# Kernel optimization log

Measured on AMD Instinct MI355X. Metric: run time of the kernel, lower is better.

Reference implementation:

```python
import jax, jax.numpy as jnp
import numpy as np
from jax import lax

NUM_TAGS = 126
T = NUM_TAGS + 2          # tag_size = 128
B, S = 256, 512
START, STOP = T - 3, T - 2
NEG = -10000.0


def setup_inputs() -> dict:
    key = jax.random.key(0)
    k1, k2, k3 = jax.random.split(key, 3)
    feats = jax.random.normal(k1, (B, S, T), jnp.float32)
    # learned transition matrix with the module's init masking pattern
    trans = jax.random.normal(k2, (T, T), jnp.float32)
    trans = trans.at[:, START].set(NEG).at[STOP, :].set(NEG)
    trans = trans.at[:, 0].set(NEG).at[0, :].set(NEG)
    # prefix masks with varying valid lengths in [S/2, S]
    lengths = jax.random.randint(k3, (B,), S // 2, S + 1)
    mask = jnp.arange(S)[None, :] < lengths[:, None]
    return {"feats": feats, "mask": mask, "transitions": trans}


def reference(feats, mask, transitions):
    # Viterbi decode (module.forward returns (None, decode_idx)).
    Bn, Sn, Tn = feats.shape
    start, stop = Tn - 3, Tn - 2
    emit = jnp.transpose(feats, (1, 0, 2))            # (S, B, T)
    m = jnp.transpose(mask.astype(jnp.int32))         # (S, B)
    lengths = mask.astype(jnp.int32).sum(axis=1)      # (B,)

    part0 = emit[0] + transitions[start][None, :]     # (B, T)

    def step(part, inp):
        e_t, m_t = inp
        # scores[t, b, i, j] = feats[t, b, j] + transitions[i, j]
        cur = part[:, :, None] + transitions[None, :, :] + e_t[:, None, :]  # (B, from, to)
        new_part = cur.max(axis=1)                                          # (B, T)
        bp = jnp.argmax(cur, axis=1).astype(jnp.int32)                      # (B, T)
        bp = jnp.where(m_t[:, None] > 0, bp, 0)
        return new_part, (new_part, bp)

    _, (hist, bps) = lax.scan(step, part0, (emit[1:], m[1:]))
    part_hist = jnp.concatenate([part0[None], hist], axis=0)                # (S, B, T)
    back_points = jnp.concatenate(
        [bps, jnp.zeros((1, Bn, Tn), jnp.int32)], axis=0)                   # (S, B, T)

    bidx = jnp.arange(Bn)
    last_pos = lengths - 1                                                  # (B,)
    last_partition = part_hist[last_pos, bidx]                              # (B, T)
    last_bp = jnp.argmax(last_partition[:, :, None] + transitions[None], axis=1)
    pointer = last_bp[:, stop].astype(jnp.int32)                            # (B,)

    # overwrite back_points at the last valid position with the final pointer
    bp_bt = jnp.transpose(back_points, (1, 0, 2))                           # (B, S, T)
    bp_bt = bp_bt.at[bidx, last_pos].set(
        jnp.broadcast_to(pointer[:, None], (Bn, Tn)))
    back_points = jnp.transpose(bp_bt, (1, 0, 2))                           # (S, B, T)

    def trace(ptr, bp_t):
        new_ptr = jnp.take_along_axis(bp_t, ptr[:, None], axis=1)[:, 0]
        return new_ptr, new_ptr

    _, rev = lax.scan(trace, pointer, back_points[:-1], reverse=True)       # (S-1, B)
    decode = jnp.concatenate([rev, pointer[None]], axis=0)                  # (S, B)
    return jnp.transpose(decode)                                            # (B, S)
```

## Files before the change

### kernel.cpp

```cpp
#include <hip/hip_runtime.h>
#include <cstdint>
#include <cstddef>

constexpr int T_ = 128;
constexpr int S_ = 512;
constexpr int B_ = 256;
constexpr int START_ = T_ - 3;
constexpr int STOP_  = T_ - 2;
constexpr float NEGINF_ = -3.402823466e38f;

__device__ __forceinline__ void lds_barrier() {
  asm volatile("s_waitcnt lgkmcnt(0)\n\ts_barrier" ::: "memory");
}

__device__ __forceinline__ float readlane_f(float v, int sl) {
  return __int_as_float(__builtin_amdgcn_readlane(__float_as_int(v), sl));
}

__device__ __forceinline__ float ig_reduce_max(float m) {
  int x = __builtin_amdgcn_mov_dpp(__float_as_int(m), 0xB1, 0xF, 0xF, true);
  m = fmaxf(m, __int_as_float(x));
  x = __builtin_amdgcn_mov_dpp(__float_as_int(m), 0x4E, 0xF, 0xF, true);
  m = fmaxf(m, __int_as_float(x));
  x = __builtin_amdgcn_mov_dpp(__float_as_int(m), 0x141, 0xF, 0xF, true);
  m = fmaxf(m, __int_as_float(x));
  return m;
}

__global__ __launch_bounds__(256) void viterbi_forward(
    const float* __restrict__ feats,
    const float* __restrict__ trans,
    float* __restrict__ ph)
{
  const int tid  = threadIdx.x;
  const int lane = tid & 63;
  const int w    = tid >> 6;
  const int ig   = lane & 7;
  const int jl   = lane >> 3;
  const int jg   = w * 8 + jl;
  const int j0   = jg * 4;
  const int b    = blockIdx.x;

  __shared__ alignas(16) float part[2][160];

  float4 tc[16];
  #pragma unroll
  for (int ii = 0; ii < 16; ++ii)
    tc[ii] = *(const float4*)&trans[(16 * ig + ii) * T_ + j0];

  const float* fb = feats + (size_t)b * S_ * T_;
  const int woff = j0 + 4 * (jg >> 2);

  float4 e0 = *(const float4*)&fb[j0];
  float4 ts = *(const float4*)&trans[START_ * T_ + j0];
  float4 p0 = make_float4(e0.x + ts.x, e0.y + ts.y, e0.z + ts.z, e0.w + ts.w);
  if (ig == 0) {
    *(float4*)&part[0][woff] = p0;
    *(float4*)&ph[(size_t)b * T_ + j0] = p0;
  }
  float4 e_next = *(const float4*)&fb[T_ + j0];
  __syncthreads();

  for (int t = 1; t < S_; ++t) {
    float4 e_cur = e_next;
    if (t + 1 < S_) e_next = *(const float4*)&fb[(size_t)(t + 1) * T_ + j0];

    const float4* p4 = (const float4*)part[(t - 1) & 1];
    float4 p[4];
    #pragma unroll
    for (int q = 0; q < 4; ++q) p[q] = p4[5 * ig + q];

    float m0 = NEGINF_, m1 = NEGINF_, m2 = NEGINF_, m3 = NEGINF_;
    #pragma unroll
    for (int q = 0; q < 4; ++q) {
      float4 pv = p[q];
      float4 t0 = tc[4 * q + 0], t1 = tc[4 * q + 1];
      float4 t2 = tc[4 * q + 2], t3 = tc[4 * q + 3];
      m0 = fmaxf(m0, fmaxf(fmaxf(pv.x + t0.x, pv.y + t1.x),
                           fmaxf(pv.z + t2.x, pv.w + t3.x)));
      m1 = fmaxf(m1, fmaxf(fmaxf(pv.x + t0.y, pv.y + t1.y),
                           fmaxf(pv.z + t2.y, pv.w + t3.y)));
      m2 = fmaxf(m2, fmaxf(fmaxf(pv.x + t0.z, pv.y + t1.z),
                           fmaxf(pv.z + t2.z, pv.w + t3.z)));
      m3 = fmaxf(m3, fmaxf(fmaxf(pv.x + t0.w, pv.y + t1.w),
                           fmaxf(pv.z + t2.w, pv.w + t3.w)));
    }
    float4 np4 = make_float4(ig_reduce_max(m0) + e_cur.x,
                             ig_reduce_max(m1) + e_cur.y,
                             ig_reduce_max(m2) + e_cur.z,
                             ig_reduce_max(m3) + e_cur.w);
    if (ig == 0) *(float4*)&part[t & 1][woff] = np4;
    lds_barrier();
    if (ig == 0)
      *(float4*)&ph[((size_t)t * B_ + b) * T_ + j0] = np4;
  }
}

constexpr int CH_ = 8;
constexpr int TS_ = 130;

__global__ __launch_bounds__(64) void viterbi_trace(
    const float* __restrict__ feats,
    const void*  __restrict__ mask,
    const float* __restrict__ trans,
    const float* __restrict__ ph,
    int* __restrict__ out)
{
  const int b    = blockIdx.x;
  const int lane = threadIdx.x;

  __shared__ alignas(16) float transT[T_ * TS_];
  #pragma unroll 4
  for (int g = lane; g < T_ * T_; g += 64) {
    int i = g >> 7, jj = g & (T_ - 1);
    transT[jj * TS_ + i] = trans[g];
  }
  __syncthreads();

  int len = 0;
  {
    const int w0 = *(const int*)mask;
    if (w0 == 0x01010101) {
      const unsigned char* m = (const unsigned char*)mask + (size_t)b * S_;
      for (int s = lane; s < S_; s += 64) len += (m[s] != 0);
    } else if (w0 == 0x3F800000) {
      const float* m = (const float*)mask + (size_t)b * S_;
      for (int s = lane; s < S_; s += 64) len += (m[s] != 0.0f);
    } else {
      const int* m = (const int*)mask + (size_t)b * S_;
      for (int s = lane; s < S_; s += 64) len += (m[s] != 0);
    }
    #pragma unroll
    for (int o = 32; o > 0; o >>= 1) len += __shfl_xor(len, o);
  }
  const int lp = len - 1;

  const float2 L = *(const float2*)(ph + ((size_t)lp * B_ + b) * T_ + 2 * lane);
  float v0 = L.x + transT[STOP_ * TS_ + 2 * lane];
  float v1 = L.y + transT[STOP_ * TS_ + 2 * lane + 1];
  float mx = fmaxf(v0, v1);
  #pragma unroll
  for (int o = 32; o > 0; o >>= 1) mx = fmaxf(mx, __shfl_xor(mx, o));
  {
    unsigned long long g0 = __ballot(v0 == mx);
    unsigned long long g1 = __ballot(v1 == mx);
    int p0 = g0 ? 2 * (__ffsll(g0) - 1)     : (1 << 30);
    int p1 = g1 ? 2 * (__ffsll(g1) - 1) + 1 : (1 << 30);
    int pointer = min(p0, p1);

    for (int k = lp + 1 + lane; k <= S_ - 2; k += 64) out[b * S_ + k] = 0;
    if (lane == 0) {
      out[b * S_ + (S_ - 1)] = pointer;
      if (lp < S_ - 1) out[b * S_ + lp] = pointer;
    }

    int   ptr = pointer;
    float tg  = readlane_f((ptr & 1) ? L.y : L.x, ptr >> 1);
    const float* fb = feats + (size_t)b * S_ * T_;
    const float2 FL = *(const float2*)(fb + (size_t)lp * T_ + 2 * lane);
    float e = readlane_f((ptr & 1) ? FL.y : FL.x, ptr >> 1);

    float2 PA[CH_], FA[CH_], PB[CH_], FB[CH_];

    auto issue = [&](float2 (&P)[CH_], float2 (&F)[CH_], int k0) {
      #pragma unroll
      for (int s = 0; s < CH_; ++s) {
        int k = k0 - s; if (k < 0) k = 0;
        P[s] = *(const float2*)(ph + ((size_t)k * B_ + b) * T_ + 2 * lane);
        F[s] = *(const float2*)(fb + (size_t)k * T_ + 2 * lane);
      }
    };
    auto process = [&](const float2 (&P)[CH_], const float2 (&F)[CH_], int k0) {
      #pragma unroll
      for (int s = 0; s < CH_; ++s) {
        const int k = k0 - s;
        if (k >= 0) {
          const float2 tr = *(const float2*)(transT + ptr * TS_ + 2 * lane);
          float cx = (P[s].x + tr.x) + e;
          float cy = (P[s].y + tr.y) + e;
          unsigned long long q0 = __ballot(cx == tg);
          unsigned long long q1 = __ballot(cy == tg);
          int a0 = q0 ? 2 * (__ffsll(q0) - 1)     : (1 << 30);
          int a1 = q1 ? 2 * (__ffsll(q1) - 1) + 1 : (1 << 30);
          ptr = min(a0, a1);
          if (lane == 0) out[b * S_ + k] = ptr;
          tg = readlane_f((ptr & 1) ? P[s].y : P[s].x, ptr >> 1);
          e  = readlane_f((ptr & 1) ? F[s].y : F[s].x, ptr >> 1);
        }
      }
    };

    issue(PA, FA, lp - 1);
    for (int k0 = lp - 1; k0 >= 0; k0 -= 2 * CH_) {
      issue(PB, FB, k0 - CH_);
      process(PA, FA, k0);
      issue(PA, FA, k0 - 2 * CH_);
      process(PB, FB, k0 - CH_);
    }
  }
}

extern "C" void kernel_launch(void* const* d_in, const int* in_sizes, int n_in,
                              void* d_out, int out_size, void* d_ws, size_t ws_size,
                              hipStream_t stream) {
  const float* feats = (const float*)d_in[0];
  const void*  mask  = d_in[1];
  const float* trans = (const float*)d_in[2];
  float* ph = (float*)d_ws;
  int*   out = (int*)d_out;

  viterbi_forward<<<dim3(B_), dim3(256), 0, stream>>>(feats, trans, ph);
  viterbi_trace  <<<dim3(B_), dim3(64), 0, stream>>>(feats, mask, trans, ph, out);
}
```

Before: 455.4 us.

## Store byte backpointers in forward pass and trace them from LDS

```diff
diff --git a/kernel.cpp b/kernel.cpp
--- a/kernel.cpp
+++ b/kernel.cpp
@@ -7,17 +7,12 @@
 constexpr int B_ = 256;
 constexpr int START_ = T_ - 3;
 constexpr int STOP_  = T_ - 2;
-constexpr float NEGINF_ = -3.402823466e38f;
 
 __device__ __forceinline__ void lds_barrier() {
   asm volatile("s_waitcnt lgkmcnt(0)\n\ts_barrier" ::: "memory");
 }
 
-__device__ __forceinline__ float readlane_f(float v, int sl) {
-  return __int_as_float(__builtin_amdgcn_readlane(__float_as_int(v), sl));
-}
-
-__device__ __forceinline__ float ig_reduce_max(float m) {
+__device__ __forceinline__ float ig_rmax(float m) {
   int x = __builtin_amdgcn_mov_dpp(__float_as_int(m), 0xB1, 0xF, 0xF, true);
   m = fmaxf(m, __int_as_float(x));
   x = __builtin_amdgcn_mov_dpp(__float_as_int(m), 0x4E, 0xF, 0xF, true);
@@ -26,12 +21,24 @@
   m = fmaxf(m, __int_as_float(x));
   return m;
 }
+__device__ __forceinline__ int ig_rmin(int m) {
+  int x = __builtin_amdgcn_mov_dpp(m, 0xB1, 0xF, 0xF, true);
+  m = min(m, x);
+  x = __builtin_amdgcn_mov_dpp(m, 0x4E, 0xF, 0xF, true);
+  m = min(m, x);
+  x = __builtin_amdgcn_mov_dpp(m, 0x141, 0xF, 0xF, true);
+  m = min(m, x);
+  return m;
+}
 
 __global__ __launch_bounds__(256) void viterbi_forward(
     const float* __restrict__ feats,
     const float* __restrict__ trans,
-    float* __restrict__ ph)
+    const void*  __restrict__ mask,
+    unsigned int* __restrict__ bp4,
+    float* __restrict__ lastpart)
 {
+  const int b    = blockIdx.x;
   const int tid  = threadIdx.x;
   const int lane = tid & 63;
   const int w    = tid >> 6;
@@ -39,83 +46,146 @@
   const int jl   = lane >> 3;
   const int jg   = w * 8 + jl;
   const int j0   = jg * 4;
-  const int b    = blockIdx.x;
+  const int ig16 = ig * 16;
 
   __shared__ alignas(16) float part[2][160];
-
-  float4 tc[16];
+  __shared__ int lensh[4];
+
+  float tcc[4][16];
   #pragma unroll
-  for (int ii = 0; ii < 16; ++ii)
-    tc[ii] = *(const float4*)&trans[(16 * ig + ii) * T_ + j0];
-
-  const float* fb = feats + (size_t)b * S_ * T_;
-  const int woff = j0 + 4 * (jg >> 2);
-
-  float4 e0 = *(const float4*)&fb[j0];
-  float4 ts = *(const float4*)&trans[START_ * T_ + j0];
-  float4 p0 = make_float4(e0.x + ts.x, e0.y + ts.y, e0.z + ts.z, e0.w + ts.w);
-  if (ig == 0) {
-    *(float4*)&part[0][woff] = p0;
-    *(float4*)&ph[(size_t)b * T_ + j0] = p0;
-  }
-  float4 e_next = *(const float4*)&fb[T_ + j0];
+  for (int ii = 0; ii < 16; ++ii) {
+    float4 v = *(const float4*)&trans[(ig16 + ii) * T_ + j0];
+    tcc[0][ii] = v.x; tcc[1][ii] = v.y; tcc[2][ii] = v.z; tcc[3][ii] = v.w;
+  }
+
+  int cnt = 0;
+  {
+    const int w0 = *(const int*)mask;
+    if (w0 == 0x01010101) {
+      const unsigned char* m = (const unsigned char*)mask + (size_t)b * S_;
+      cnt = (m[tid] != 0) + (m[tid + 256] != 0);
+    } else if (w0 == 0x3F800000) {
+      const float* m = (const float*)mask + (size_t)b * S_;
+      cnt = (m[tid] != 0.0f) + (m[tid + 256] != 0.0f);
+    } else {
+      const int* m = (const int*)mask + (size_t)b * S_;
+      cnt = (m[tid] != 0) + (m[tid + 256] != 0);
+    }
+    #pragma unroll
+    for (int o = 32; o > 0; o >>= 1) cnt += __shfl_xor(cnt, o);
+    if (lane == 0) lensh[w] = cnt;
+  }
+
+  const float* fb   = feats + (size_t)b * S_ * T_;
+  const int    woff = j0 + 4 * (jg >> 2);
+
+  float4 e0v = *(const float4*)&fb[j0];
+  float4 tsv = *(const float4*)&trans[START_ * T_ + j0];
+  float4 p0  = {e0v.x + tsv.x, e0v.y + tsv.y, e0v.z + tsv.z, e0v.w + tsv.w};
+  if (ig == 0) *(float4*)&part[0][woff] = p0;
   __syncthreads();
-
-  for (int t = 1; t < S_; ++t) {
-    float4 e_cur = e_next;
-    if (t + 1 < S_) e_next = *(const float4*)&fb[(size_t)(t + 1) * T_ + j0];
-
+  const int lp = lensh[0] + lensh[1] + lensh[2] + lensh[3] - 1;
+
+  auto stepf = [&](int t, float4 e4) {
     const float4* p4 = (const float4*)part[(t - 1) & 1];
-    float4 p[4];
-    #pragma unroll
-    for (int q = 0; q < 4; ++q) p[q] = p4[5 * ig + q];
-
-    float m0 = NEGINF_, m1 = NEGINF_, m2 = NEGINF_, m3 = NEGINF_;
+    float pp[16];
     #pragma unroll
     for (int q = 0; q < 4; ++q) {
-      float4 pv = p[q];
-      float4 t0 = tc[4 * q + 0], t1 = tc[4 * q + 1];
-      float4 t2 = tc[4 * q + 2], t3 = tc[4 * q + 3];
-      m0 = fmaxf(m0, fmaxf(fmaxf(pv.x + t0.x, pv.y + t1.x),
-                           fmaxf(pv.z + t2.x, pv.w + t3.x)));
-      m1 = fmaxf(m1, fmaxf(fmaxf(pv.x + t0.y, pv.y + t1.y),
-                           fmaxf(pv.z + t2.y, pv.w + t3.y)));
-      m2 = fmaxf(m2, fmaxf(fmaxf(pv.x + t0.z, pv.y + t1.z),
-                           fmaxf(pv.z + t2.z, pv.w + t3.z)));
-      m3 = fmaxf(m3, fmaxf(fmaxf(pv.x + t0.w, pv.y + t1.w),
-                           fmaxf(pv.z + t2.w, pv.w + t3.w)));
-    }
-    float4 np4 = make_float4(ig_reduce_max(m0) + e_cur.x,
-                             ig_reduce_max(m1) + e_cur.y,
-                             ig_reduce_max(m2) + e_cur.z,
-                             ig_reduce_max(m3) + e_cur.w);
+      float4 v = p4[5 * ig + q];
+      pp[4*q] = v.x; pp[4*q+1] = v.y; pp[4*q+2] = v.z; pp[4*q+3] = v.w;
+    }
+    const float ev[4] = {e4.x, e4.y, e4.z, e4.w};
+    float np[4]; int bpk[4];
+    #pragma unroll
+    for (int c = 0; c < 4; ++c) {
+      float v8[8]; int i8[8];
+      #pragma unroll
+      for (int a = 0; a < 8; ++a) {
+        float da = (pp[2*a]     + tcc[c][2*a])     + ev[c];
+        float db = (pp[2*a + 1] + tcc[c][2*a + 1]) + ev[c];
+        bool s = da >= db;
+        v8[a] = s ? da : db; i8[a] = s ? (2*a) : (2*a + 1);
+      }
+      float v4[4]; int i4[4];
+      #pragma unroll
+      for (int a = 0; a < 4; ++a) {
+        bool s = v8[2*a] >= v8[2*a + 1];
+        v4[a] = s ? v8[2*a] : v8[2*a + 1]; i4[a] = s ? i8[2*a] : i8[2*a + 1];
+      }
+      float v2[2]; int i2[2];
+      #pragma unroll
+      for (int a = 0; a < 2; ++a) {
+        bool s = v2[0] >= 0;
+        (void)s;
+        bool ss = v4[2*a] >= v4[2*a + 1];
+        v2[a] = ss ? v4[2*a] : v4[2*a + 1]; i2[a] = ss ? i4[2*a] : i4[2*a + 1];
+      }
+      bool s0 = v2[0] >= v2[1];
+      float cv = s0 ? v2[0] : v2[1];
+      int   ci = s0 ? i2[0] : i2[1];
+      float M = ig_rmax(cv);
+      int key = (cv == M) ? (ig16 + ci) : 255;
+      key = ig_rmin(key);
+      np[c] = M; bpk[c] = key;
+    }
+    float4 np4 = {np[0], np[1], np[2], np[3]};
     if (ig == 0) *(float4*)&part[t & 1][woff] = np4;
     lds_barrier();
-    if (ig == 0)
-      *(float4*)&ph[((size_t)t * B_ + b) * T_ + j0] = np4;
-  }
-}
-
-constexpr int CH_ = 8;
-constexpr int TS_ = 130;
+    if (ig == 0) {
+      unsigned pk = (unsigned)bpk[0] | ((unsigned)bpk[1] << 8) |
+                    ((unsigned)bpk[2] << 16) | ((unsigned)bpk[3] << 24);
+      bp4[(size_t)(b * S_ + (t - 1)) * 32 + jg] = pk;
+      if (t == lp) *(float4*)&lastpart[b * T_ + j0] = np4;
+    }
+  };
+
+  float4 EA[4], EB[4];
+  #pragma unroll
+  for (int u = 0; u < 4; ++u)
+    EA[u] = *(const float4*)&fb[(size_t)(1 + u) * T_ + j0];
+
+  for (int t0 = 1; t0 < S_; t0 += 8) {
+    #pragma unroll
+    for (int u = 0; u < 4; ++u) {
+      int tr = t0 + 4 + u; tr = tr > S_ - 1 ? S_ - 1 : tr;
+      EB[u] = *(const float4*)&fb[(size_t)tr * T_ + j0];
+    }
+    #pragma unroll
+    for (int u = 0; u < 4; ++u) { int t = t0 + u; if (t < S_) stepf(t, EA[u]); }
+    #pragma unroll
+    for (int u = 0; u < 4; ++u) {
+      int tr = t0 + 8 + u; tr = tr > S_ - 1 ? S_ - 1 : tr;
+      EA[u] = *(const float4*)&fb[(size_t)tr * T_ + j0];
+    }
+    #pragma unroll
+    for (int u = 0; u < 4; ++u) { int t = t0 + 4 + u; if (t < S_) stepf(t, EB[u]); }
+  }
+}
 
 __global__ __launch_bounds__(64) void viterbi_trace(
-    const float* __restrict__ feats,
+    const float* __restrict__ trans,
     const void*  __restrict__ mask,
-    const float* __restrict__ trans,
-    const float* __restrict__ ph,
+    const unsigned char* __restrict__ bp,
+    const float* __restrict__ lastpart,
     int* __restrict__ out)
 {
   const int b    = blockIdx.x;
   const int lane = threadIdx.x;
 
-  __shared__ alignas(16) float transT[T_ * TS_];
-  #pragma unroll 4
-  for (int g = lane; g < T_ * T_; g += 64) {
-    int i = g >> 7, jj = g & (T_ - 1);
-    transT[jj * TS_ + i] = trans[g];
-  }
-  __syncthreads();
+  __shared__ unsigned char bplds[S_ * T_];
+
+  {
+    const uint4* g = (const uint4*)(bp + (size_t)b * S_ * T_);
+    uint4* l = (uint4*)bplds;
+    #pragma unroll
+    for (int r = 0; r < 64; r += 8) {
+      uint4 v[8];
+      #pragma unroll
+      for (int q = 0; q < 8; ++q) v[q] = g[(r + q) * 64 + lane];
+      #pragma unroll
+      for (int q = 0; q < 8; ++q) l[(r + q) * 64 + lane] = v[q];
+    }
+  }
 
   int len = 0;
   {
@@ -135,67 +205,32 @@
   }
   const int lp = len - 1;
 
-  const float2 L = *(const float2*)(ph + ((size_t)lp * B_ + b) * T_ + 2 * lane);
-  float v0 = L.x + transT[STOP_ * TS_ + 2 * lane];
-  float v1 = L.y + transT[STOP_ * TS_ + 2 * lane + 1];
+  const float2 L = *(const float2*)(lastpart + b * T_ + 2 * lane);
+  float tr0 = trans[(2 * lane) * T_ + STOP_];
+  float tr1 = trans[(2 * lane + 1) * T_ + STOP_];
+  float v0 = L.x + tr0, v1 = L.y + tr1;
   float mx = fmaxf(v0, v1);
   #pragma unroll
   for (int o = 32; o > 0; o >>= 1) mx = fmaxf(mx, __shfl_xor(mx, o));
-  {
-    unsigned long long g0 = __ballot(v0 == mx);
-    unsigned long long g1 = __ballot(v1 == mx);
-    int p0 = g0 ? 2 * (__ffsll(g0) - 1)     : (1 << 30);
-    int p1 = g1 ? 2 * (__ffsll(g1) - 1) + 1 : (1 << 30);
-    int pointer = min(p0, p1);
-
-    for (int k = lp + 1 + lane; k <= S_ - 2; k += 64) out[b * S_ + k] = 0;
-    if (lane == 0) {
-      out[b * S_ + (S_ - 1)] = pointer;
-      if (lp < S_ - 1) out[b * S_ + lp] = pointer;
-    }
-
-    int   ptr = pointer;
-    float tg  = readlane_f((ptr & 1) ? L.y : L.x, ptr >> 1);
-    const float* fb = feats + (size_t)b * S_ * T_;
-    const float2 FL = *(const float2*)(fb + (size_t)lp * T_ + 2 * lane);
-    float e = readlane_f((ptr & 1) ? FL.y : FL.x, ptr >> 1);
-
-    float2 PA[CH_], FA[CH_], PB[CH_], FB[CH_];
-
-    auto issue = [&](float2 (&P)[CH_], float2 (&F)[CH_], int k0) {
-      #pragma unroll
-      for (int s = 0; s < CH_; ++s) {
-        int k = k0 - s; if (k < 0) k = 0;
-        P[s] = *(const float2*)(ph + ((size_t)k * B_ + b) * T_ + 2 * lane);
-        F[s] = *(const float2*)(fb + (size_t)k * T_ + 2 * lane);
-      }
-    };
-    auto process = [&](const float2 (&P)[CH_], const float2 (&F)[CH_], int k0) {
-      #pragma unroll
-      for (int s = 0; s < CH_; ++s) {
-        const int k = k0 - s;
-        if (k >= 0) {
-          const float2 tr = *(const float2*)(transT + ptr * TS_ + 2 * lane);
-          float cx = (P[s].x + tr.x) + e;
-          float cy = (P[s].y + tr.y) + e;
-          unsigned long long q0 = __ballot(cx == tg);
-          unsigned long long q1 = __ballot(cy == tg);
-          int a0 = q0 ? 2 * (__ffsll(q0) - 1)     : (1 << 30);
-          int a1 = q1 ? 2 * (__ffsll(q1) - 1) + 1 : (1 << 30);
-          ptr = min(a0, a1);
-          if (lane == 0) out[b * S_ + k] = ptr;
-          tg = readlane_f((ptr & 1) ? P[s].y : P[s].x, ptr >> 1);
-          e  = readlane_f((ptr & 1) ? F[s].y : F[s].x, ptr >> 1);
-        }
-      }
-    };
-
-    issue(PA, FA, lp - 1);
-    for (int k0 = lp - 1; k0 >= 0; k0 -= 2 * CH_) {
-      issue(PB, FB, k0 - CH_);
-      process(PA, FA, k0);
-      issue(PA, FA, k0 - 2 * CH_);
-      process(PB, FB, k0 - CH_);
+  unsigned long long g0 = __ballot(v0 == mx);
+  unsigned long long g1 = __ballot(v1 == mx);
+  int p0 = g0 ? 2 * (__ffsll(g0) - 1)     : (1 << 30);
+  int p1 = g1 ? 2 * (__ffsll(g1) - 1) + 1 : (1 << 30);
+  const int pointer = min(p0, p1);
+
+  for (int k = lp + 1 + lane; k <= S_ - 2; k += 64) out[b * S_ + k] = 0;
+  if (lane == 0) {
+    out[b * S_ + (S_ - 1)] = pointer;
+    if (lp < S_ - 1) out[b * S_ + lp] = pointer;
+  }
+
+  __syncthreads();
+
+  if (lane == 0) {
+    int ptr = pointer;
+    for (int k = lp - 1; k >= 0; --k) {
+      ptr = bplds[k * T_ + ptr];
+      out[b * S_ + k] = ptr;
     }
   }
 }
@@ -206,9 +241,13 @@
   const float* feats = (const float*)d_in[0];
   const void*  mask  = d_in[1];
   const float* trans = (const float*)d_in[2];
-  float* ph = (float*)d_ws;
-  int*   out = (int*)d_out;
-
-  viterbi_forward<<<dim3(B_), dim3(256), 0, stream>>>(feats, trans, ph);
-  viterbi_trace  <<<dim3(B_), dim3(64), 0, stream>>>(feats, mask, trans, ph, out);
-}
+  int* out = (int*)d_out;
+
+  unsigned char* bp = (unsigned char*)d_ws;
+  float* lastpart = (float*)((char*)d_ws + (size_t)B_ * S_ * T_);
+
+  viterbi_forward<<<dim3(B_), dim3(256), 0, stream>>>(
+      feats, trans, mask, (unsigned int*)bp, lastpart);
+  viterbi_trace<<<dim3(B_), dim3(64), 0, stream>>>(
+      trans, mask, bp, lastpart, out);
+}
```

After: 591.0 us. +29.8%, slower.
